# Kernel tuning notes

Measured on AMD Instinct MI355X. Metric: run time of the kernel, lower is better.

## Reference

```python
import jax, jax.numpy as jnp
import numpy as np

H = 512   # hidden_size
IN = 5    # input_size
OUT = 2   # output_size
B = 2048
T_HIST = 50


def _lstm_cell(x, h, c, W_ih, W_hh, b_ih, b_hh):
    # PyTorch gate order: i, f, g, o
    z = x @ W_ih.T + h @ W_hh.T + (b_ih + b_hh)
    i, f, g, o = jnp.split(z, 4, axis=-1)
    i = jax.nn.sigmoid(i)
    f = jax.nn.sigmoid(f)
    g = jnp.tanh(g)
    o = jax.nn.sigmoid(o)
    c2 = f * c + i * g
    h2 = o * jnp.tanh(c2)
    return h2, c2


def setup_inputs() -> dict:
    key = jax.random.key(0)
    ks = jax.random.split(key, 20)
    s = 0.05
    inp = {
        "history": jax.random.normal(ks[0], (B, T_HIST, IN), dtype=jnp.float32),
        "future_frames": 30,
        # encoder layer 0 (input IN) and layer 1 (input H)
        "enc_W_ih0": jax.random.normal(ks[1], (4 * H, IN)) * s,
        "enc_W_hh0": jax.random.normal(ks[2], (4 * H, H)) * s,
        "enc_b_ih0": jnp.zeros((4 * H,), jnp.float32),
        "enc_b_hh0": jnp.zeros((4 * H,), jnp.float32),
        "enc_W_ih1": jax.random.normal(ks[3], (4 * H, H)) * s,
        "enc_W_hh1": jax.random.normal(ks[4], (4 * H, H)) * s,
        "enc_b_ih1": jnp.zeros((4 * H,), jnp.float32),
        "enc_b_hh1": jnp.zeros((4 * H,), jnp.float32),
        # decoder layer 0 (input OUT) and layer 1 (input H)
        "dec_W_ih0": jax.random.normal(ks[5], (4 * H, OUT)) * s,
        "dec_W_hh0": jax.random.normal(ks[6], (4 * H, H)) * s,
        "dec_b_ih0": jnp.zeros((4 * H,), jnp.float32),
        "dec_b_hh0": jnp.zeros((4 * H,), jnp.float32),
        "dec_W_ih1": jax.random.normal(ks[7], (4 * H, H)) * s,
        "dec_W_hh1": jax.random.normal(ks[8], (4 * H, H)) * s,
        "dec_b_ih1": jnp.zeros((4 * H,), jnp.float32),
        "dec_b_hh1": jnp.zeros((4 * H,), jnp.float32),
        # output head
        "out_W": jax.random.normal(ks[9], (OUT, H)) * s,
        "out_b": jnp.zeros((OUT,), jnp.float32),
    }
    return inp


def reference(history, enc_W_ih0, enc_W_hh0, enc_b_ih0, enc_b_hh0,
              enc_W_ih1, enc_W_hh1, enc_b_ih1, enc_b_hh1,
              dec_W_ih0, dec_W_hh0, dec_b_ih0, dec_b_hh0,
              dec_W_ih1, dec_W_hh1, dec_b_ih1, dec_b_hh1,
              out_W, out_b, future_frames):
    batch = history.shape[0]
    z = jnp.zeros((batch, H), history.dtype)

    # ----- encoder: 2-layer LSTM over history, scan over time -----
    def enc_step(carry, x_t):
        h0, c0, h1, c1 = carry
        h0, c0 = _lstm_cell(x_t, h0, c0, enc_W_ih0, enc_W_hh0, enc_b_ih0, enc_b_hh0)
        h1, c1 = _lstm_cell(h0, h1, c1, enc_W_ih1, enc_W_hh1, enc_b_ih1, enc_b_hh1)
        return (h0, c0, h1, c1), None

    xs = jnp.swapaxes(history, 0, 1)  # [T, B, IN]
    (h0, c0, h1, c1), _ = jax.lax.scan(enc_step, (z, z, z, z), xs)

    def dec_step(carry, _):
        h0, c0, h1, c1, x_prev = carry
        h0, c0 = _lstm_cell(x_prev, h0, c0, dec_W_ih0, dec_W_hh0, dec_b_ih0, dec_b_hh0)
        h1, c1 = _lstm_cell(h0, h1, c1, dec_W_ih1, dec_W_hh1, dec_b_ih1, dec_b_hh1)
        pred = h1 @ out_W.T + out_b  # [B, OUT]
        return (h0, c0, h1, c1, pred), pred

    x0 = jnp.zeros((batch, OUT), history.dtype)
    _, preds = jax.lax.scan(dec_step, (h0, c0, h1, c1, x0), None, length=future_frames)
    return jnp.swapaxes(preds, 0, 1)  # [B, T_fut, OUT]
```

## Files before the change

### kernel.cpp

```cpp
#include <hip/hip_runtime.h>
#include <hip/hip_bf16.h>


#define HDIM 512
#define BDIM 2048
#define T_HIST 50
#define T_FUT 30

typedef __attribute__((ext_vector_type(8))) short short8;
typedef __attribute__((ext_vector_type(4))) float f32x4;

#define AS1(p) ((const __attribute__((address_space(1))) void*)(p))
#define AS3(p) ((__attribute__((address_space(3))) void*)(p))

__device__ __forceinline__ ushort f2bf(float f) {
    union { float f; unsigned u; } v; v.f = f;
    unsigned r = v.u + 0x7fff + ((v.u >> 16) & 1);
    return (ushort)(r >> 16);
}
__device__ __forceinline__ float bf2f(ushort h) {
    union { unsigned u; float f; } v; v.u = ((unsigned)h) << 16;
    return v.f;
}

__device__ __forceinline__ int swz(int row, int slot) {
    int q = row >> 1;
    int t = ((row & 1) << 2) | slot;
    return q * 8 + (t ^ (q & 7));
}

struct SplitSrc { const float* src[6]; };

__global__ __launch_bounds__(256) void split_weights(SplitSrc s, ushort* __restrict__ hi,
                                                     ushort* __restrict__ lo) {
    int row = blockIdx.x;
    int j = blockIdx.y;
    int g = row >> 9, u = row & 511;
    int rp = (u >> 5) * 128 + ((u >> 4) & 1) * 64 + g * 16 + (u & 15);
    const float* S = s.src[j] + (size_t)row * HDIM;
    ushort* H = hi + ((size_t)j * 2048 + rp) * HDIM;
    ushort* L = lo + ((size_t)j * 2048 + rp) * HDIM;
    for (int k = threadIdx.x; k < HDIM; k += 256) {
        float w = S[k];
        ushort hb = f2bf(w);
        H[k] = hb;
        L[k] = f2bf(w - bf2f(hb));
    }
}

struct CellDesc {
    const ushort *A1h, *A1l, *W1h, *W1l;
    const ushort *A2h, *A2l, *W2h, *W2l;
    const float *x; const float *Wx;
    const float *bih, *bhh;
    const ushort *hsrc_hi, *hsrc_lo;
    const float *Wout, *bout; float *out_t;
    float* c; ushort *hh; ushort *hl;
    int np, xs, Kx;
};

template <bool HF>
__global__ __launch_bounds__(256, 2) void lstm_cells(CellDesc dA, CellDesc dB) {
    __shared__ __align__(16) ushort lds[2 * 16384];

    const CellDesc d = (blockIdx.x >> 8) ? dB : dA;

    const int tid = threadIdx.x;
    const int w = tid >> 6, l = tid & 63;
    const int wm = w >> 1, wn = w & 1;
    const int lrow = l & 15, lk = l >> 4;

    int id = blockIdx.x & 255;
    int xcd = id & 7, rr = id >> 3;
    int bx = (xcd & 3) * 4 + (rr & 3);
    int by = (xcd >> 2) * 8 + (rr >> 2);
    const int m0 = by * 128;
    const int n0 = bx * 128;
    const int u  = bx * 32 + wn * 16 + lrow;

    f32x4 acc[4][4];

    auto STAGE = [&](int t) {
        int buf = t & 1;
        int p = t >> 4;
        int kc = (t & 15) * 32;
        const ushort* Ah = p ? d.A2h : d.A1h;
        const ushort* Al = p ? d.A2l : d.A1l;
        const ushort* Bh = p ? d.W2h : d.W1h;
        const ushort* Bl = p ? d.W2l : d.W1l;
        ushort* base = &lds[buf * 16384];
        #pragma unroll
        for (int it = 0; it < 2; ++it) {
            int db = (w * 2 + it) * 64;
            int dd = db + l;
            int q = dd >> 3, tp = dd & 7;
            int tl = tp ^ (q & 7);
            int r = (q << 1) | (tl >> 2);
            int s = tl & 3;
            size_t go = (size_t)r * HDIM + kc + s * 8;
            __builtin_amdgcn_global_load_lds(AS1(Ah + (size_t)m0 * HDIM + go),
                                             AS3(base + db * 8), 16, 0, 0);
            __builtin_amdgcn_global_load_lds(AS1(Al + (size_t)m0 * HDIM + go),
                                             AS3(base + 4096 + db * 8), 16, 0, 0);
            __builtin_amdgcn_global_load_lds(AS1(Bh + (size_t)n0 * HDIM + go),
                                             AS3(base + 8192 + db * 8), 16, 0, 0);
            __builtin_amdgcn_global_load_lds(AS1(Bl + (size_t)n0 * HDIM + go),
                                             AS3(base + 12288 + db * 8), 16, 0, 0);
        }
    };

    const int nch = d.np * 16;
    STAGE(0);

    #pragma unroll
    for (int g = 0; g < 4; ++g) {
        float b = d.bih[g * HDIM + u] + d.bhh[g * HDIM + u];
        f32x4 bv = {b, b, b, b};
        #pragma unroll
        for (int fm = 0; fm < 4; ++fm) acc[fm][g] = bv;
    }

    if (d.Kx > 0) {
        for (int kx = 0; kx < d.Kx; ++kx) {
            float wv[4];
            #pragma unroll
            for (int g = 0; g < 4; ++g) wv[g] = d.Wx[(size_t)(g * HDIM + u) * d.Kx + kx];
            #pragma unroll
            for (int fm = 0; fm < 4; ++fm)
                #pragma unroll
                for (int r = 0; r < 4; ++r) {
                    int m = m0 + wm * 64 + fm * 16 + lk * 4 + r;
                    float xv = d.x[(size_t)m * d.xs + kx];
                    #pragma unroll
                    for (int g = 0; g < 4; ++g) acc[fm][g][r] += xv * wv[g];
                }
        }
    }

    if constexpr (HF) {
        __shared__ float xlds[128][2];
        if (d.hsrc_hi) {
            int row = tid >> 1, half = tid & 1;
            const ushort* hh = d.hsrc_hi + (size_t)(m0 + row) * HDIM + half * 256;
            const ushort* hl = d.hsrc_lo + (size_t)(m0 + row) * HDIM + half * 256;
            float s0 = 0.f, s1 = 0.f;
            #pragma unroll 4
            for (int j = 0; j < 32; ++j) {
                short8 a = *(const short8*)(hh + j * 8);
                short8 b = *(const short8*)(hl + j * 8);
                #pragma unroll
                for (int e = 0; e < 8; ++e) {
                    float hv = bf2f((ushort)a[e]) + bf2f((ushort)b[e]);
                    int k = half * 256 + j * 8 + e;
                    s0 += hv * d.Wout[k];
                    s1 += hv * d.Wout[HDIM + k];
                }
            }
            s0 += __shfl_xor(s0, 1);
            s1 += __shfl_xor(s1, 1);
            float x0 = s0 + d.bout[0], x1 = s1 + d.bout[1];
            if (half == 0) {
                xlds[row][0] = x0; xlds[row][1] = x1;
                if (bx == 0 && d.out_t) {
                    d.out_t[(size_t)(m0 + row) * (T_FUT * 2) + 0] = x0;
                    d.out_t[(size_t)(m0 + row) * (T_FUT * 2) + 1] = x1;
                }
            }
            __syncthreads();
            #pragma unroll
            for (int g = 0; g < 4; ++g) {
                float w0 = d.Wx[(size_t)(g * HDIM + u) * 2 + 0];
                float w1 = d.Wx[(size_t)(g * HDIM + u) * 2 + 1];
                #pragma unroll
                for (int fm = 0; fm < 4; ++fm)
                    #pragma unroll
                    for (int r = 0; r < 4; ++r) {
                        int ml = wm * 64 + fm * 16 + lk * 4 + r;
                        acc[fm][g][r] += xlds[ml][0] * w0 + xlds[ml][1] * w1;
                    }
            }
        }
    }

    for (int t = 0; t < nch; ++t) {
        __syncthreads();
        if (t + 1 < nch) STAGE(t + 1);
        ushort* base = &lds[(t & 1) * 16384];
        short8 ah[4], al[4], bh[4], bl[4];
        #pragma unroll
        for (int fm = 0; fm < 4; ++fm) {
            int row = wm * 64 + fm * 16 + lrow;
            int off = swz(row, lk) * 8;
            ah[fm] = *(const short8*)(base + off);
            al[fm] = *(const short8*)(base + 4096 + off);
        }
        #pragma unroll
        for (int g = 0; g < 4; ++g) {
            int row = wn * 64 + g * 16 + lrow;
            int off = swz(row, lk) * 8;
            bh[g] = *(const short8*)(base + 8192 + off);
            bl[g] = *(const short8*)(base + 12288 + off);
        }
        #pragma unroll
        for (int fm = 0; fm < 4; ++fm)
            #pragma unroll
            for (int g = 0; g < 4; ++g)
                acc[fm][g] = __builtin_amdgcn_mfma_f32_16x16x32_bf16(
                    ah[fm], bh[g], acc[fm][g], 0, 0, 0);
        #pragma unroll
        for (int fm = 0; fm < 4; ++fm)
            #pragma unroll
            for (int g = 0; g < 4; ++g)
                acc[fm][g] = __builtin_amdgcn_mfma_f32_16x16x32_bf16(
                    al[fm], bh[g], acc[fm][g], 0, 0, 0);
        #pragma unroll
        for (int fm = 0; fm < 4; ++fm)
            #pragma unroll
            for (int g = 0; g < 4; ++g)
                acc[fm][g] = __builtin_amdgcn_mfma_f32_16x16x32_bf16(
                    ah[fm], bl[g], acc[fm][g], 0, 0, 0);
    }

    #pragma unroll
    for (int fm = 0; fm < 4; ++fm)
        #pragma unroll
        for (int r = 0; r < 4; ++r) {
            int m = m0 + wm * 64 + fm * 16 + lk * 4 + r;
            size_t idx = (size_t)m * HDIM + u;
            float zi = acc[fm][0][r], zf = acc[fm][1][r];
            float zg = acc[fm][2][r], zo = acc[fm][3][r];
            float ig = 1.f / (1.f + __expf(-zi));
            float fg = 1.f / (1.f + __expf(-zf));
            float gg = 2.f / (1.f + __expf(-2.f * zg)) - 1.f;
            float og = 1.f / (1.f + __expf(-zo));
            float cn = fg * d.c[idx] + ig * gg;
            float hn = og * (2.f / (1.f + __expf(-2.f * cn)) - 1.f);
            d.c[idx] = cn;
            ushort hb = f2bf(hn);
            d.hh[idx] = hb;
            d.hl[idx] = f2bf(hn - bf2f(hb));
        }
}

__global__ __launch_bounds__(256) void head_kernel(
    const ushort* __restrict__ hhi, const ushort* __restrict__ hlo,
    const float* __restrict__ Wout, const float* __restrict__ bout,
    float* __restrict__ out, int t)
{
    int wave = (blockIdx.x * 256 + threadIdx.x) >> 6;
    int lane = threadIdx.x & 63;
    const ushort* hr = hhi + (size_t)wave * HDIM;
    const ushort* lr = hlo + (size_t)wave * HDIM;
    float s0 = 0.f, s1 = 0.f;
    #pragma unroll
    for (int k = lane; k < HDIM; k += 64) {
        float hv = bf2f(hr[k]) + bf2f(lr[k]);
        s0 += hv * Wout[k];
        s1 += hv * Wout[HDIM + k];
    }
    #pragma unroll
    for (int off = 32; off > 0; off >>= 1) {
        s0 += __shfl_down(s0, off);
        s1 += __shfl_down(s1, off);
    }
    if (lane == 0) {
        out[(size_t)wave * (T_FUT * 2) + t * 2 + 0] = s0 + bout[0];
        out[(size_t)wave * (T_FUT * 2) + t * 2 + 1] = s1 + bout[1];
    }
}

extern "C" void kernel_launch(void* const* d_in, const int* in_sizes, int n_in,
                              void* d_out, int out_size, void* d_ws, size_t ws_size,
                              hipStream_t stream) {
    const float* history = (const float*)d_in[0];
    const float* eWih0 = (const float*)d_in[2];
    const float* eWhh0 = (const float*)d_in[3];
    const float* ebih0 = (const float*)d_in[4];
    const float* ebhh0 = (const float*)d_in[5];
    const float* eWih1 = (const float*)d_in[6];
    const float* eWhh1 = (const float*)d_in[7];
    const float* ebih1 = (const float*)d_in[8];
    const float* ebhh1 = (const float*)d_in[9];
    const float* dWih0 = (const float*)d_in[10];
    const float* dWhh0 = (const float*)d_in[11];
    const float* dbih0 = (const float*)d_in[12];
    const float* dbhh0 = (const float*)d_in[13];
    const float* dWih1 = (const float*)d_in[14];
    const float* dWhh1 = (const float*)d_in[15];
    const float* dbih1 = (const float*)d_in[16];
    const float* dbhh1 = (const float*)d_in[17];
    const float* outW  = (const float*)d_in[18];
    const float* outb  = (const float*)d_in[19];
    float* out = (float*)d_out;

    const size_t M = (size_t)2048 * 512;
    ushort* whi = (ushort*)d_ws;
    ushort* wlo = whi + 6 * M;
    ushort* hb  = wlo + 6 * M;
    float*  c0  = (float*)(hb + 8 * M);
    float*  c1  = c0 + M;

    ushort* h0a_hi = hb + 0 * M; ushort* h0a_lo = hb + 1 * M;
    ushort* h0b_hi = hb + 2 * M; ushort* h0b_lo = hb + 3 * M;
    ushort* h1a_hi = hb + 4 * M; ushort* h1a_lo = hb + 5 * M;
    ushort* h1b_hi = hb + 6 * M; ushort* h1b_lo = hb + 7 * M;

    hipMemsetAsync(h0a_hi, 0, 2 * M * sizeof(ushort), stream);
    hipMemsetAsync(h1a_hi, 0, 2 * M * sizeof(ushort), stream);
    hipMemsetAsync(c0, 0, 2 * M * sizeof(float), stream);

    SplitSrc ss;
    ss.src[0] = eWhh0; ss.src[1] = eWih1; ss.src[2] = eWhh1;
    ss.src[3] = dWhh0; ss.src[4] = dWih1; ss.src[5] = dWhh1;
    split_weights<<<dim3(2048, 6), 256, 0, stream>>>(ss, whi, wlo);

    #define WHI(j) (whi + (size_t)(j) * M)
    #define WLO(j) (wlo + (size_t)(j) * M)

    auto H0R_HI = [&](int s){ return (s & 1) ? h0b_hi : h0a_hi; };
    auto H0R_LO = [&](int s){ return (s & 1) ? h0b_lo : h0a_lo; };
    auto H0W_HI = [&](int s){ return (s & 1) ? h0a_hi : h0b_hi; };
    auto H0W_LO = [&](int s){ return (s & 1) ? h0a_lo : h0b_lo; };
    auto H1R_HI = [&](int s){ return (s & 1) ? h1b_hi : h1a_hi; };
    auto H1R_LO = [&](int s){ return (s & 1) ? h1b_lo : h1a_lo; };
    auto H1W_HI = [&](int s){ return (s & 1) ? h1a_hi : h1b_hi; };
    auto H1W_LO = [&](int s){ return (s & 1) ? h1a_lo : h1b_lo; };

    auto mkL0enc = [&](int s) {
        CellDesc d{};
        d.A1h = H0R_HI(s); d.A1l = H0R_LO(s); d.W1h = WHI(0); d.W1l = WLO(0);
        d.np = 1; d.x = history + s * 5; d.xs = T_HIST * 5; d.Kx = 5; d.Wx = eWih0;
        d.bih = ebih0; d.bhh = ebhh0; d.c = c0; d.hh = H0W_HI(s); d.hl = H0W_LO(s);
        return d;
    };
    auto mkL1enc = [&](int s) {
        CellDesc d{};
        d.A1h = H0W_HI(s); d.A1l = H0W_LO(s); d.W1h = WHI(1); d.W1l = WLO(1);
        d.A2h = H1R_HI(s); d.A2l = H1R_LO(s); d.W2h = WHI(2); d.W2l = WLO(2);
        d.np = 2; d.Kx = 0; d.xs = 0;
        d.bih = ebih1; d.bhh = ebhh1; d.c = c1; d.hh = H1W_HI(s); d.hl = H1W_LO(s);
        return d;
    };
    auto mkD0 = [&](int s) {
        CellDesc d{};
        d.A1h = H0R_HI(s); d.A1l = H0R_LO(s); d.W1h = WHI(3); d.W1l = WLO(3);
        d.np = 1; d.Kx = 0; d.xs = 0; d.Wx = dWih0;
        if (s > T_HIST) {
            d.hsrc_hi = H1W_HI(s - 1); d.hsrc_lo = H1W_LO(s - 1);
            d.Wout = outW; d.bout = outb;
            d.out_t = out + (size_t)(s - T_HIST - 1) * 2;
        }
        d.bih = dbih0; d.bhh = dbhh0; d.c = c0; d.hh = H0W_HI(s); d.hl = H0W_LO(s);
        return d;
    };
    auto mkD1 = [&](int s) {
        CellDesc d{};
        d.A1h = H0W_HI(s); d.A1l = H0W_LO(s); d.W1h = WHI(4); d.W1l = WLO(4);
        d.A2h = H1R_HI(s); d.A2l = H1R_LO(s); d.W2h = WHI(5); d.W2l = WLO(5);
        d.np = 2; d.Kx = 0; d.xs = 0;
        d.bih = dbih1; d.bhh = dbhh1; d.c = c1; d.hh = H1W_HI(s); d.hl = H1W_LO(s);
        return d;
    };

    dim3 blk(256);

    {
        CellDesc d = mkL0enc(0);
        lstm_cells<false><<<256, blk, 0, stream>>>(d, d);
    }
    for (int s = 0; s < T_HIST; ++s) {
        CellDesc dL1 = mkL1enc(s);
        CellDesc dNx = (s + 1 < T_HIST) ? mkL0enc(s + 1) : mkD0(T_HIST);
        lstm_cells<false><<<512, blk, 0, stream>>>(dL1, dNx);
    }
    for (int s = T_HIST; s < T_HIST + T_FUT; ++s) {
        CellDesc d1 = mkD1(s);
        lstm_cells<false><<<256, blk, 0, stream>>>(d1, d1);
        if (s + 1 < T_HIST + T_FUT) {
            CellDesc d0 = mkD0(s + 1);
            lstm_cells<true><<<256, blk, 0, stream>>>(d0, d0);
        }
    }
    head_kernel<<<512, blk, 0, stream>>>(
        H1W_HI(T_HIST + T_FUT - 1), H1W_LO(T_HIST + T_FUT - 1),
        outW, outb, out, T_FUT - 1);
    #undef WHI
    #undef WLO
}
```

Measured before the change: 4.174 ms.

## Triple-buffer activation tiles and replace syncthreads with explicit vmcnt waits

```diff
diff --git a/kernel.cpp b/kernel.cpp
--- a/kernel.cpp
+++ b/kernel.cpp
@@ -61,7 +61,7 @@
 
 template <bool HF>
 __global__ __launch_bounds__(256, 2) void lstm_cells(CellDesc dA, CellDesc dB) {
-    __shared__ __align__(16) ushort lds[2 * 16384];
+    __shared__ __align__(16) ushort lds[40960];
 
     const CellDesc d = (blockIdx.x >> 8) ? dB : dA;
 
@@ -80,37 +80,52 @@
 
     f32x4 acc[4][4];
 
-    auto STAGE = [&](int t) {
-        int buf = t & 1;
+    int dbs[2]; size_t gos[2];
+    #pragma unroll
+    for (int it = 0; it < 2; ++it) {
+        int db = (w * 2 + it) * 64;
+        int dd = db + l;
+        int q = dd >> 3, tp = dd & 7;
+        int tl = tp ^ (q & 7);
+        int r = (q << 1) | (tl >> 2);
+        int s = tl & 3;
+        dbs[it] = db;
+        gos[it] = (size_t)r * HDIM + s * 8;
+    }
+
+    auto STAGE_A = [&](int t, int bufk) {
         int p = t >> 4;
         int kc = (t & 15) * 32;
-        const ushort* Ah = p ? d.A2h : d.A1h;
-        const ushort* Al = p ? d.A2l : d.A1l;
-        const ushort* Bh = p ? d.W2h : d.W1h;
-        const ushort* Bl = p ? d.W2l : d.W1l;
-        ushort* base = &lds[buf * 16384];
+        const ushort* Ah = (p ? d.A2h : d.A1h) + (size_t)m0 * HDIM + kc;
+        const ushort* Al = (p ? d.A2l : d.A1l) + (size_t)m0 * HDIM + kc;
+        ushort* base = &lds[bufk * 8192];
         #pragma unroll
         for (int it = 0; it < 2; ++it) {
-            int db = (w * 2 + it) * 64;
-            int dd = db + l;
-            int q = dd >> 3, tp = dd & 7;
-            int tl = tp ^ (q & 7);
-            int r = (q << 1) | (tl >> 2);
-            int s = tl & 3;
-            size_t go = (size_t)r * HDIM + kc + s * 8;
-            __builtin_amdgcn_global_load_lds(AS1(Ah + (size_t)m0 * HDIM + go),
-                                             AS3(base + db * 8), 16, 0, 0);
-            __builtin_amdgcn_global_load_lds(AS1(Al + (size_t)m0 * HDIM + go),
-                                             AS3(base + 4096 + db * 8), 16, 0, 0);
-            __builtin_amdgcn_global_load_lds(AS1(Bh + (size_t)n0 * HDIM + go),
-                                             AS3(base + 8192 + db * 8), 16, 0, 0);
-            __builtin_amdgcn_global_load_lds(AS1(Bl + (size_t)n0 * HDIM + go),
-                                             AS3(base + 12288 + db * 8), 16, 0, 0);
+            __builtin_amdgcn_global_load_lds(AS1(Ah + gos[it]),
+                                             AS3(base + dbs[it] * 8), 16, 0, 0);
+            __builtin_amdgcn_global_load_lds(AS1(Al + gos[it]),
+                                             AS3(base + 4096 + dbs[it] * 8), 16, 0, 0);
+        }
+    };
+    auto STAGE_B = [&](int t) {
+        int p = t >> 4;
+        int kc = (t & 15) * 32;
+        const ushort* Bh = (p ? d.W2h : d.W1h) + (size_t)n0 * HDIM + kc;
+        const ushort* Bl = (p ? d.W2l : d.W1l) + (size_t)n0 * HDIM + kc;
+        ushort* base = &lds[24576 + (t & 1) * 8192];
+        #pragma unroll
+        for (int it = 0; it < 2; ++it) {
+            __builtin_amdgcn_global_load_lds(AS1(Bh + gos[it]),
+                                             AS3(base + dbs[it] * 8), 16, 0, 0);
+            __builtin_amdgcn_global_load_lds(AS1(Bl + gos[it]),
+                                             AS3(base + 4096 + dbs[it] * 8), 16, 0, 0);
         }
     };
 
     const int nch = d.np * 16;
-    STAGE(0);
+    STAGE_B(0);
+    STAGE_A(0, 0);
+    STAGE_A(1, 1);
 
     #pragma unroll
     for (int g = 0; g < 4; ++g) {
@@ -182,24 +197,33 @@
         }
     }
 
+    int ca = 0;
     for (int t = 0; t < nch; ++t) {
-        __syncthreads();
-        if (t + 1 < nch) STAGE(t + 1);
-        ushort* base = &lds[(t & 1) * 16384];
+        if (t + 1 < nch) {
+            asm volatile("s_waitcnt vmcnt(4)" ::: "memory");
+        } else {
+            asm volatile("s_waitcnt vmcnt(0)" ::: "memory");
+        }
+        __builtin_amdgcn_s_barrier();
+        if (t + 1 < nch) STAGE_B(t + 1);
+        if (t + 2 < nch) STAGE_A(t + 2, ca == 0 ? 2 : ca - 1);
+
+        ushort* abase = &lds[ca * 8192];
+        ushort* bbase = &lds[24576 + (t & 1) * 8192];
         short8 ah[4], al[4], bh[4], bl[4];
         #pragma unroll
         for (int fm = 0; fm < 4; ++fm) {
             int row = wm * 64 + fm * 16 + lrow;
             int off = swz(row, lk) * 8;
-            ah[fm] = *(const short8*)(base + off);
-            al[fm] = *(const short8*)(base + 4096 + off);
+            ah[fm] = *(const short8*)(abase + off);
+            al[fm] = *(const short8*)(abase + 4096 + off);
         }
         #pragma unroll
         for (int g = 0; g < 4; ++g) {
             int row = wn * 64 + g * 16 + lrow;
             int off = swz(row, lk) * 8;
-            bh[g] = *(const short8*)(base + 8192 + off);
-            bl[g] = *(const short8*)(base + 12288 + off);
+            bh[g] = *(const short8*)(bbase + off);
+            bl[g] = *(const short8*)(bbase + 4096 + off);
         }
         #pragma unroll
         for (int fm = 0; fm < 4; ++fm)
@@ -219,6 +243,8 @@
             for (int g = 0; g < 4; ++g)
                 acc[fm][g] = __builtin_amdgcn_mfma_f32_16x16x32_bf16(
                     ah[fm], bl[g], acc[fm][g], 0, 0, 0);
+
+        ca = (ca == 2) ? 0 : ca + 1;
     }
 
     #pragma unroll
```

Result: no change. 4.252 ms (+1.9%).
